# Kernel tuning notes

Hardware: AMD Instinct MI355X
Metric: run time of the kernel (lower is better)

## Reference

```python
import jax, jax.numpy as jnp
import numpy as np
from jax import lax

BETA = 0.95
THRESH = 1.0
NUM_INPUTS, NUM_HIDDEN, NUM_CLASSES, NUM_STEPS, BATCH = 80, 256, 2, 200, 4096


@jax.custom_vjp
def spike_fn(x):
    # Heaviside spike; surrogate gradient = fast_sigmoid (slope=25)
    return (x > 0).astype(x.dtype)

def _spike_fwd(x):
    return spike_fn(x), x

def _spike_bwd(x, g):
    slope = 25.0
    return (g / (slope * jnp.abs(x) + 1.0) ** 2,)

spike_fn.defvjp(_spike_fwd, _spike_bwd)


def _linear_init(key, fan_in, fan_out):
    # torch nn.Linear default init: U(-1/sqrt(fan_in), 1/sqrt(fan_in))
    k1, k2 = jax.random.split(key)
    bound = 1.0 / np.sqrt(fan_in)
    W = jax.random.uniform(k1, (fan_out, fan_in), jnp.float32, -bound, bound)
    b = jax.random.uniform(k2, (fan_out,), jnp.float32, -bound, bound)
    return W, b


def setup_inputs() -> dict:
    key = jax.random.key(0)
    kx, k1, k2, k3, k4 = jax.random.split(key, 5)
    x = jax.random.normal(kx, (BATCH, NUM_INPUTS, NUM_STEPS), jnp.float32)
    W1, b1 = _linear_init(k1, NUM_INPUTS, NUM_HIDDEN)
    W2, b2 = _linear_init(k2, NUM_HIDDEN, NUM_HIDDEN)
    W3, b3 = _linear_init(k3, NUM_HIDDEN, NUM_HIDDEN)
    W4, b4 = _linear_init(k4, NUM_HIDDEN, NUM_CLASSES)
    return {"x": x, "W1": W1, "b1": b1, "W2": W2, "b2": b2,
            "W3": W3, "b3": b3, "W4": W4, "b4": b4}


def _lif(cur, mem):
    # snntorch Leaky, reset_mechanism='subtract': reset from previous mem (detached)
    reset = lax.stop_gradient((mem > THRESH).astype(mem.dtype))
    mem = BETA * mem + cur - reset * THRESH
    spk = spike_fn(mem - THRESH)
    return spk, mem


def reference(x, W1, b1, W2, b2, W3, b3, W4, b4):
    B = x.shape[0]
    xt = jnp.transpose(x, (2, 0, 1))  # [T, B, 80]
    m1 = jnp.zeros((B, NUM_HIDDEN), x.dtype)
    m2 = jnp.zeros((B, NUM_HIDDEN), x.dtype)
    m3 = jnp.zeros((B, NUM_HIDDEN), x.dtype)
    m4 = jnp.zeros((B, NUM_CLASSES), x.dtype)

    def step(carry, x_t):
        m1, m2, m3, m4 = carry
        s1, m1 = _lif(x_t @ W1.T + b1, m1)
        s2, m2 = _lif(s1 @ W2.T + b2, m2)
        s3, m3 = _lif(s2 @ W3.T + b3, m3)
        s4, m4 = _lif(s3 @ W4.T + b4, m4)
        return (m1, m2, m3, m4), s4

    _, spk4_rec = lax.scan(step, (m1, m2, m3, m4), xt)
    return spk4_rec  # [T, B, num_classes]
```

## Files before the change

kernel.cpp:

```cpp
#include <hip/hip_runtime.h>
#include <cstddef>


#define BATCH 4096
#define TSTEPS 200
#define NIN 80
#define KP 96
#define NH 256
#define XPAD 104
#define SPAD 264
#define WP1 104

#define W1HI 0
#define W1LO 24576
#define W2HI 49152
#define W2LO 114688
#define W3HI 180224
#define W3LO 245760

#define LO_SCALE 2048.0f
#define LO_INV 4.8828125e-4f

typedef _Float16 h8 __attribute__((ext_vector_type(8)));
typedef float f4 __attribute__((ext_vector_type(4)));

__device__ __forceinline__ void lds_barrier() {
  __builtin_amdgcn_s_waitcnt(0xC07F);
  __builtin_amdgcn_s_barrier();
}

__device__ __forceinline__ void pin4(f4& v) { asm volatile("" : "+a"(v)); }
__device__ __forceinline__ void pinh(h8& v) { asm volatile("" : "+a"(v)); }

__global__ __launch_bounds__(256) void prep_kernel(
    const float* __restrict__ W1, const float* __restrict__ W2,
    const float* __restrict__ W3, _Float16* __restrict__ ws) {
  unsigned id = blockIdx.x * 256u + threadIdx.x;
  if (id >= 24576u + 65536u + 65536u) return;
  float v;
  unsigned off;
  _Float16 *hi, *lo;
  if (id < 24576u) {
    unsigned n = id / KP, k = id % KP;
    v = (k < NIN) ? W1[n * NIN + k] : 0.0f;
    hi = ws + W1HI; lo = ws + W1LO; off = id;
  } else if (id < 90112u) {
    off = id - 24576u; v = W2[off];
    hi = ws + W2HI; lo = ws + W2LO;
  } else {
    off = id - 90112u; v = W3[off];
    hi = ws + W3HI; lo = ws + W3LO;
  }
  _Float16 h = (_Float16)v;
  float r = (v - (float)h) * LO_SCALE;
  hi[off] = h;
  lo[off] = (_Float16)r;
}

__global__ __attribute__((amdgpu_waves_per_eu(4, 4)))
__launch_bounds__(1024) void snn_kernel(
    const float* __restrict__ x,
    const float* __restrict__ b1, const float* __restrict__ b2,
    const float* __restrict__ b3, const float* __restrict__ W4,
    const float* __restrict__ b4, const _Float16* __restrict__ ws,
    float* __restrict__ out) {
  __shared__ alignas(16) _Float16 Wl1[256][WP1];
  __shared__ alignas(16) _Float16 xAhi[8][16][XPAD];
  __shared__ alignas(16) _Float16 xAlo[8][16][XPAD];
  __shared__ alignas(16) _Float16 S1[16][SPAD];
  __shared__ alignas(16) _Float16 S2[16][SPAD];
  __shared__ alignas(16) _Float16 S3[16][SPAD];

  const int tid = threadIdx.x;
  const int wave = tid >> 6;
  const int lane = tid & 63;
  const int n16 = lane & 15;
  const int kg = lane >> 4;
  const int wb = blockIdx.x << 4;
  const int nn = (wave << 4) + n16;

  for (int c = tid; c < 3072; c += 1024) {
    int row = c / 12, w = c % 12;
    *(h8*)&Wl1[row][w * 8] = *(const h8*)(ws + W1LO + row * KP + w * 8);
  }

  h8 w1h[3];
  {
    const _Float16* w1p = ws + W1HI + nn * KP;
#pragma unroll
    for (int kt = 0; kt < 3; ++kt)
      w1h[kt] = *(const h8*)(w1p + kt * 32 + kg * 8);
#pragma unroll
    for (int kt = 0; kt < 3; ++kt) pinh(w1h[kt]);
  }

  const _Float16* w2l = ws + W2LO + nn * NH;
  const _Float16* w3l = ws + W3LO + nn * NH;

  const float bb1 = b1[nn], bb2 = b2[nn], bb3 = b3[nn];

  f4 w2hi_f[8], w3hi_f[8];
  {
    const float* w2h = (const float*)(ws + W2HI + nn * NH);
    const float* w3h = (const float*)(ws + W3HI + nn * NH);
#pragma unroll
    for (int kt = 0; kt < 8; ++kt) {
      w2hi_f[kt] = *(const f4*)(w2h + kt * 16 + kg * 4);
      w3hi_f[kt] = *(const f4*)(w3h + kt * 16 + kg * 4);
    }
#pragma unroll
    for (int kt = 0; kt < 8; ++kt) {
      pin4(w2hi_f[kt]);
      pin4(w3hi_f[kt]);
    }
  }

  const int j4 = lane >> 5;
  const int ks4 = (lane & 31) << 3;
  const float* w4p = W4 + j4 * NH + ks4;
  const float bb4 = b4[j4];

  float mem1[4] = {0.f, 0.f, 0.f, 0.f};
  float mem2[4] = {0.f, 0.f, 0.f, 0.f};
  float mem3[4] = {0.f, 0.f, 0.f, 0.f};
  float mem4 = 0.f;

  for (int t = 0; t < TSTEPS; ++t) {
    const int ph = t & 7;
    if (ph == 0) {
      for (unsigned e = (unsigned)tid; e < 3072u; e += 1024u) {
        unsigned m = e / 192u, r = e % 192u, i = r >> 1, t4 = r & 1u;
        f4 v = {0.f, 0.f, 0.f, 0.f};
        if (i < NIN)
          v = *(const f4*)(x + ((size_t)(wb + m) * NIN + i) * TSTEPS + t +
                           t4 * 4);
#pragma unroll
        for (int s = 0; s < 4; ++s) {
          float f = v[s];
          _Float16 h = (_Float16)f;
          xAhi[t4 * 4 + s][m][i] = h;
          xAlo[t4 * 4 + s][m][i] = (_Float16)((f - (float)h) * LO_SCALE);
        }
      }
      lds_barrier();
    }

    h8 wl2a[4];
#pragma unroll
    for (int q = 0; q < 4; ++q)
      wl2a[q] = *(const h8*)(w2l + q * 32 + kg * 8);

    f4 aH = {0.f, 0.f, 0.f, 0.f};
    f4 aL = {0.f, 0.f, 0.f, 0.f};
#pragma unroll
    for (int kt = 0; kt < 3; ++kt) {
      const int ko = kt * 32 + kg * 8;
      h8 ahi = *(const h8*)&xAhi[ph][n16][ko];
      h8 alo = *(const h8*)&xAlo[ph][n16][ko];
      h8 wl = *(const h8*)&Wl1[nn][ko];
      aH = __builtin_amdgcn_mfma_f32_16x16x32_f16(ahi, w1h[kt], aH, 0, 0, 0);
      aL = __builtin_amdgcn_mfma_f32_16x16x32_f16(alo, w1h[kt], aL, 0, 0, 0);
      aL = __builtin_amdgcn_mfma_f32_16x16x32_f16(ahi, wl, aL, 0, 0, 0);
    }
#pragma unroll
    for (int r = 0; r < 4; ++r) {
      float cur = __fadd_rn(__fadd_rn(aH[r], __fmul_rn(aL[r], LO_INV)), bb1);
      float mo = mem1[r];
      float mn = __fsub_rn(__fadd_rn(__fmul_rn(0.95f, mo), cur),
                           (mo > 1.0f) ? 1.0f : 0.0f);
      mem1[r] = mn;
      S1[kg * 4 + r][nn] = (mn > 1.0f) ? (_Float16)1.0f : (_Float16)0.0f;
    }
    lds_barrier();

    h8 wl2b[4];
#pragma unroll
    for (int q = 0; q < 4; ++q)
      wl2b[q] = *(const h8*)(w2l + (4 + q) * 32 + kg * 8);

    aH = (f4){0.f, 0.f, 0.f, 0.f};
    aL = (f4){0.f, 0.f, 0.f, 0.f};
#pragma unroll
    for (int kt = 0; kt < 8; ++kt) {
      h8 a = *(const h8*)&S1[n16][kt * 32 + kg * 8];
      aH = __builtin_amdgcn_mfma_f32_16x16x32_f16(
          a, __builtin_bit_cast(h8, w2hi_f[kt]), aH, 0, 0, 0);
    }
#pragma unroll
    for (int q = 0; q < 4; ++q) {
      h8 a = *(const h8*)&S1[n16][q * 32 + kg * 8];
      aL = __builtin_amdgcn_mfma_f32_16x16x32_f16(a, wl2a[q], aL, 0, 0, 0);
    }
    h8 wl3a[4];
#pragma unroll
    for (int q = 0; q < 4; ++q)
      wl3a[q] = *(const h8*)(w3l + q * 32 + kg * 8);
#pragma unroll
    for (int q = 0; q < 4; ++q) {
      h8 a = *(const h8*)&S1[n16][(4 + q) * 32 + kg * 8];
      aL = __builtin_amdgcn_mfma_f32_16x16x32_f16(a, wl2b[q], aL, 0, 0, 0);
    }
#pragma unroll
    for (int r = 0; r < 4; ++r) {
      float cur = __fadd_rn(__fadd_rn(aH[r], __fmul_rn(aL[r], LO_INV)), bb2);
      float mo = mem2[r];
      float mn = __fsub_rn(__fadd_rn(__fmul_rn(0.95f, mo), cur),
                           (mo > 1.0f) ? 1.0f : 0.0f);
      mem2[r] = mn;
      S2[kg * 4 + r][nn] = (mn > 1.0f) ? (_Float16)1.0f : (_Float16)0.0f;
    }
    lds_barrier();

    h8 wl3b[4];
#pragma unroll
    for (int q = 0; q < 4; ++q)
      wl3b[q] = *(const h8*)(w3l + (4 + q) * 32 + kg * 8);

    aH = (f4){0.f, 0.f, 0.f, 0.f};
    aL = (f4){0.f, 0.f, 0.f, 0.f};
#pragma unroll
    for (int kt = 0; kt < 8; ++kt) {
      h8 a = *(const h8*)&S2[n16][kt * 32 + kg * 8];
      aH = __builtin_amdgcn_mfma_f32_16x16x32_f16(
          a, __builtin_bit_cast(h8, w3hi_f[kt]), aH, 0, 0, 0);
    }
#pragma unroll
    for (int q = 0; q < 4; ++q) {
      h8 a = *(const h8*)&S2[n16][q * 32 + kg * 8];
      aL = __builtin_amdgcn_mfma_f32_16x16x32_f16(a, wl3a[q], aL, 0, 0, 0);
    }
    f4 w4a = *(const f4*)(w4p);
    f4 w4b = *(const f4*)(w4p + 4);
#pragma unroll
    for (int q = 0; q < 4; ++q) {
      h8 a = *(const h8*)&S2[n16][(4 + q) * 32 + kg * 8];
      aL = __builtin_amdgcn_mfma_f32_16x16x32_f16(a, wl3b[q], aL, 0, 0, 0);
    }
#pragma unroll
    for (int r = 0; r < 4; ++r) {
      float cur = __fadd_rn(__fadd_rn(aH[r], __fmul_rn(aL[r], LO_INV)), bb3);
      float mo = mem3[r];
      float mn = __fsub_rn(__fadd_rn(__fmul_rn(0.95f, mo), cur),
                           (mo > 1.0f) ? 1.0f : 0.0f);
      mem3[r] = mn;
      S3[kg * 4 + r][nn] = (mn > 1.0f) ? (_Float16)1.0f : (_Float16)0.0f;
    }
    lds_barrier();

    {
      h8 s = *(const h8*)&S3[wave][ks4];
      float p = 0.0f;
#pragma unroll
      for (int u = 0; u < 4; ++u)
        p = __fadd_rn(p, __fmul_rn((float)s[u], w4a[u]));
#pragma unroll
      for (int u = 0; u < 4; ++u)
        p = __fadd_rn(p, __fmul_rn((float)s[4 + u], w4b[u]));
#pragma unroll
      for (int msk = 1; msk <= 16; msk <<= 1)
        p = __fadd_rn(p, __shfl_xor(p, msk));
      float cur = __fadd_rn(p, bb4);
      float mo = mem4;
      float mn = __fsub_rn(__fadd_rn(__fmul_rn(0.95f, mo), cur),
                           (mo > 1.0f) ? 1.0f : 0.0f);
      mem4 = mn;
      if ((lane & 31) == 0)
        __builtin_nontemporal_store(
            (mn > 1.0f) ? 1.0f : 0.0f,
            out + (size_t)t * (BATCH * 2) + (size_t)(wb + wave) * 2 + j4);
    }
  }
}

extern "C" void kernel_launch(void* const* d_in, const int* in_sizes, int n_in,
                              void* d_out, int out_size, void* d_ws,
                              size_t ws_size, hipStream_t stream) {
  const float* x  = (const float*)d_in[0];
  const float* W1 = (const float*)d_in[1];
  const float* b1 = (const float*)d_in[2];
  const float* W2 = (const float*)d_in[3];
  const float* b2 = (const float*)d_in[4];
  const float* W3 = (const float*)d_in[5];
  const float* b3 = (const float*)d_in[6];
  const float* W4 = (const float*)d_in[7];
  const float* b4 = (const float*)d_in[8];
  float* out = (float*)d_out;
  _Float16* ws = (_Float16*)d_ws;

  hipLaunchKernelGGL(prep_kernel, dim3(608), dim3(256), 0, stream,
                     W1, W2, W3, ws);
  hipLaunchKernelGGL(snn_kernel, dim3(BATCH / 16), dim3(1024), 0, stream,
                     x, b1, b2, b3, W4, b4, ws, out);
}
```

Measured before the change: 2.580 ms.

## Stream W2/W3 high weights from global each step instead of pinning in AGPRs

Stops holding the W1, W2 and W3 high-half weight fragments in registers pinned to AGPRs. The W1 high half now sits in shared memory and the W1 low half is read from global memory. The W2 and W3 high halves are reloaded from global (L2/L1) on every timestep. This frees a large block of registers, but adds global loads inside the serial time loop. The nontemporal output store also becomes a plain store.

```diff
diff --git a/kernel.cpp b/kernel.cpp
--- a/kernel.cpp
+++ b/kernel.cpp
@@ -28,9 +28,6 @@
   __builtin_amdgcn_s_waitcnt(0xC07F);
   __builtin_amdgcn_s_barrier();
 }
-
-__device__ __forceinline__ void pin4(f4& v) { asm volatile("" : "+a"(v)); }
-__device__ __forceinline__ void pinh(h8& v) { asm volatile("" : "+a"(v)); }
 
 __global__ __launch_bounds__(256) void prep_kernel(
     const float* __restrict__ W1, const float* __restrict__ W2,
@@ -64,7 +61,7 @@
     const float* __restrict__ b3, const float* __restrict__ W4,
     const float* __restrict__ b4, const _Float16* __restrict__ ws,
     float* __restrict__ out) {
-  __shared__ alignas(16) _Float16 Wl1[256][WP1];
+  __shared__ alignas(16) _Float16 Wh1[256][WP1];
   __shared__ alignas(16) _Float16 xAhi[8][16][XPAD];
   __shared__ alignas(16) _Float16 xAlo[8][16][XPAD];
   __shared__ alignas(16) _Float16 S1[16][SPAD];
@@ -81,39 +78,16 @@
 
   for (int c = tid; c < 3072; c += 1024) {
     int row = c / 12, w = c % 12;
-    *(h8*)&Wl1[row][w * 8] = *(const h8*)(ws + W1LO + row * KP + w * 8);
+    *(h8*)&Wh1[row][w * 8] = *(const h8*)(ws + W1HI + row * KP + w * 8);
   }
 
-  h8 w1h[3];
-  {
-    const _Float16* w1p = ws + W1HI + nn * KP;
-#pragma unroll
-    for (int kt = 0; kt < 3; ++kt)
-      w1h[kt] = *(const h8*)(w1p + kt * 32 + kg * 8);
-#pragma unroll
-    for (int kt = 0; kt < 3; ++kt) pinh(w1h[kt]);
-  }
-
+  const _Float16* w1l = ws + W1LO + nn * KP;
+  const _Float16* w2h = ws + W2HI + nn * NH;
   const _Float16* w2l = ws + W2LO + nn * NH;
+  const _Float16* w3h = ws + W3HI + nn * NH;
   const _Float16* w3l = ws + W3LO + nn * NH;
 
   const float bb1 = b1[nn], bb2 = b2[nn], bb3 = b3[nn];
-
-  f4 w2hi_f[8], w3hi_f[8];
-  {
-    const float* w2h = (const float*)(ws + W2HI + nn * NH);
-    const float* w3h = (const float*)(ws + W3HI + nn * NH);
-#pragma unroll
-    for (int kt = 0; kt < 8; ++kt) {
-      w2hi_f[kt] = *(const f4*)(w2h + kt * 16 + kg * 4);
-      w3hi_f[kt] = *(const f4*)(w3h + kt * 16 + kg * 4);
-    }
-#pragma unroll
-    for (int kt = 0; kt < 8; ++kt) {
-      pin4(w2hi_f[kt]);
-      pin4(w3hi_f[kt]);
-    }
-  }
 
   const int j4 = lane >> 5;
   const int ks4 = (lane & 31) << 3;
@@ -145,6 +119,11 @@
       lds_barrier();
     }
 
+    h8 w1lo[3];
+#pragma unroll
+    for (int kt = 0; kt < 3; ++kt)
+      w1lo[kt] = *(const h8*)(w1l + kt * 32 + kg * 8);
+
     h8 wl2a[4];
 #pragma unroll
     for (int q = 0; q < 4; ++q)
@@ -157,10 +136,10 @@
       const int ko = kt * 32 + kg * 8;
       h8 ahi = *(const h8*)&xAhi[ph][n16][ko];
       h8 alo = *(const h8*)&xAlo[ph][n16][ko];
-      h8 wl = *(const h8*)&Wl1[nn][ko];
-      aH = __builtin_amdgcn_mfma_f32_16x16x32_f16(ahi, w1h[kt], aH, 0, 0, 0);
-      aL = __builtin_amdgcn_mfma_f32_16x16x32_f16(alo, w1h[kt], aL, 0, 0, 0);
-      aL = __builtin_amdgcn_mfma_f32_16x16x32_f16(ahi, wl, aL, 0, 0, 0);
+      h8 wh = *(const h8*)&Wh1[nn][ko];
+      aH = __builtin_amdgcn_mfma_f32_16x16x32_f16(ahi, wh, aH, 0, 0, 0);
+      aL = __builtin_amdgcn_mfma_f32_16x16x32_f16(alo, wh, aL, 0, 0, 0);
+      aL = __builtin_amdgcn_mfma_f32_16x16x32_f16(ahi, w1lo[kt], aL, 0, 0, 0);
     }
 #pragma unroll
     for (int r = 0; r < 4; ++r) {
@@ -182,9 +161,9 @@
     aL = (f4){0.f, 0.f, 0.f, 0.f};
 #pragma unroll
     for (int kt = 0; kt < 8; ++kt) {
+      h8 w = *(const h8*)(w2h + kt * 32 + kg * 8);
       h8 a = *(const h8*)&S1[n16][kt * 32 + kg * 8];
-      aH = __builtin_amdgcn_mfma_f32_16x16x32_f16(
-          a, __builtin_bit_cast(h8, w2hi_f[kt]), aH, 0, 0, 0);
+      aH = __builtin_amdgcn_mfma_f32_16x16x32_f16(a, w, aH, 0, 0, 0);
     }
 #pragma unroll
     for (int q = 0; q < 4; ++q) {
@@ -220,9 +199,9 @@
     aL = (f4){0.f, 0.f, 0.f, 0.f};
 #pragma unroll
     for (int kt = 0; kt < 8; ++kt) {
+      h8 w = *(const h8*)(w3h + kt * 32 + kg * 8);
       h8 a = *(const h8*)&S2[n16][kt * 32 + kg * 8];
-      aH = __builtin_amdgcn_mfma_f32_16x16x32_f16(
-          a, __builtin_bit_cast(h8, w3hi_f[kt]), aH, 0, 0, 0);
+      aH = __builtin_amdgcn_mfma_f32_16x16x32_f16(a, w, aH, 0, 0, 0);
     }
 #pragma unroll
     for (int q = 0; q < 4; ++q) {
@@ -265,9 +244,8 @@
                            (mo > 1.0f) ? 1.0f : 0.0f);
       mem4 = mn;
       if ((lane & 31) == 0)
-        __builtin_nontemporal_store(
-            (mn > 1.0f) ? 1.0f : 0.0f,
-            out + (size_t)t * (BATCH * 2) + (size_t)(wb + wave) * 2 + j4);
+        out[(size_t)t * (BATCH * 2) + (size_t)(wb + wave) * 2 + j4] =
+            (mn > 1.0f) ? 1.0f : 0.0f;
     }
   }
 }
```

New measurement: 2.715 ms. +5.3%, slower.
